# Optimization experiments

Hardware: AMD Instinct MI355X
Metric: run time of the kernel (lower is better)

Reference implementation:

```python
import jax, jax.numpy as jnp
import numpy as np

N = 50000      # nodes
E = 800000     # edges
IN_DIM = 256
H = 128
OUT_DIM = 64
DEPTH = 3
NEG_SLOPE = 0.2  # DGL GATConv default leaky_relu slope


def setup_inputs() -> dict:
    key = jax.random.key(0)
    ks = jax.random.split(key, 20)
    def nrm(k, shape, fan_in):
        return jax.random.normal(k, shape, jnp.float32) / jnp.sqrt(jnp.float32(fan_in))
    x = jax.random.normal(ks[0], (N, IN_DIM), jnp.float32)
    src = jax.random.randint(ks[1], (E,), 0, N, jnp.int32)
    dst = jax.random.randint(ks[2], (E,), 0, N, jnp.int32)
    # weights stored as [in, out] (y = x @ W + b)
    inp = dict(
        x=x, src=src, dst=dst,
        wx_W=nrm(ks[3], (IN_DIM, H), IN_DIM), wx_b=jnp.zeros((H,), jnp.float32),
        gat_W=nrm(ks[4], (DEPTH, H, H), H), gat_b=jnp.zeros((DEPTH, H), jnp.float32),
        attn_l=nrm(ks[5], (DEPTH, H), H), attn_r=nrm(ks[6], (DEPTH, H), H),
        ig_W=nrm(ks[7], (DEPTH, 2 * H, H), 2 * H), ig_b=jnp.zeros((DEPTH, H), jnp.float32),
        fg_W=nrm(ks[8], (DEPTH, 2 * H, H), 2 * H), fg_b=jnp.zeros((DEPTH, H), jnp.float32),
        og_W=nrm(ks[9], (DEPTH, 2 * H, H), 2 * H), og_b=jnp.zeros((DEPTH, H), jnp.float32),
        st_W=nrm(ks[10], (DEPTH, 2 * H, H), 2 * H), st_b=jnp.zeros((DEPTH, H), jnp.float32),
        out_W=nrm(ks[11], (H, OUT_DIM), H), out_b=jnp.zeros((OUT_DIM,), jnp.float32),
    )
    return inp


def _breadth(h, W, b, a_l, a_r, src, dst):
    """DGL GATConv with 1 head + tanh activation; mean over heads is identity."""
    z = h @ W                                  # [N, H]
    el = z @ a_l                               # [N]
    er = z @ a_r                               # [N]
    e = jax.nn.leaky_relu(el[src] + er[dst], NEG_SLOPE)   # [E]
    # edge softmax over incoming edges of each dst node
    emax = jax.ops.segment_max(e, dst, num_segments=N)    # [N]
    emax = jnp.where(jnp.isfinite(emax), emax, 0.0)       # guard isolated nodes
    ex = jnp.exp(e - emax[dst])                            # [E]
    denom = jax.ops.segment_sum(ex, dst, num_segments=N)   # [N]
    alpha = ex / jnp.maximum(denom, 1e-16)[dst]             # [E]
    agg = jax.ops.segment_sum(alpha[:, None] * z[src], dst, num_segments=N)  # [N, H]
    return jnp.tanh(agg + b)


def reference(x, src, dst, wx_W, wx_b, gat_W, gat_b, attn_l, attn_r,
              ig_W, ig_b, fg_W, fg_b, og_W, og_b, st_W, st_b, out_W, out_b):
    h0 = x @ wx_W + wx_b                       # [N, H]
    h = h0
    collector = []
    for i in range(DEPTH):
        h = _breadth(h, gat_W[i], gat_b[i], attn_l[i], attn_r[i], src, dst)
        collector.append(h)
    mu = h0
    c = jnp.zeros_like(mu)
    for i in range(DEPTH):
        hm = jnp.concatenate([collector[i], mu], axis=1)   # [N, 2H]
        ig = jax.nn.sigmoid(hm @ ig_W[i] + ig_b[i])
        fg = jax.nn.sigmoid(hm @ fg_W[i] + fg_b[i])
        og = jax.nn.sigmoid(hm @ og_W[i] + og_b[i])
        c_tilde = jnp.tanh(hm @ st_W[i] + st_b[i])
        c = fg * c + ig * c_tilde
        mu = og * jnp.tanh(c)
    return jax.nn.relu(mu @ out_W + out_b)     # [N, OUT_DIM]
```

## Files before the change

kernel.cpp:

```cpp
#include <hip/hip_runtime.h>
#include <math.h>
#include <type_traits>

#define NN 50000
#define EE 800000
#define IN_D 256
#define HH 128
#define OUT_D 64
#define DEPTH 3
#define BK 512
#define NBK 98

typedef unsigned short u16;
typedef __bf16  bf16x8 __attribute__((ext_vector_type(8)));
typedef short   short8 __attribute__((ext_vector_type(8)));
typedef float   f32x4  __attribute__((ext_vector_type(4)));

__device__ __forceinline__ u16 f2b(float f){
    unsigned u = __float_as_uint(f);
    u += 0x7fff + ((u>>16)&1);
    return (u16)(u>>16);
}
__device__ __forceinline__ float b2f(u16 h){ return __uint_as_float(((unsigned)h)<<16); }

#define LOG2E 1.4426950408889634f
#if __has_builtin(__builtin_amdgcn_exp2f)
__device__ __forceinline__ float fexp2(float x){ return __builtin_amdgcn_exp2f(x); }
#else
__device__ __forceinline__ float fexp2(float x){ return exp2f(x); }
#endif
#if __has_builtin(__builtin_amdgcn_rcpf)
__device__ __forceinline__ float frcp(float x){ return __builtin_amdgcn_rcpf(x); }
#else
__device__ __forceinline__ float frcp(float x){ return 1.f/x; }
#endif
__device__ __forceinline__ float sigm(float x){ return frcp(1.f + fexp2(-x*LOG2E)); }
__device__ __forceinline__ float ftanh(float x){
    float ax = fabsf(x);
    float u = fexp2(ax * (-2.f*LOG2E));
    float r = (1.f - u) * frcp(1.f + u);
    return copysignf(r, x);
}

enum { EPI_BF=0, EPI_RELU=1, EPI_ZEL=2 };

template<int EPI, int WAVES, int CT, int K, typename TA>
__global__ __launch_bounds__(WAVES*64, 4) void rgemm_k(
    const TA* __restrict__ A1,
    const u16* __restrict__ Bp,
    const float* __restrict__ b1, const float* __restrict__ b2,
    void* __restrict__ Out, float* __restrict__ aux1, float* __restrict__ aux2,
    int Nrows)
{
    constexpr int TH = WAVES*64;
    constexpr int KS = K/32;
    constexpr int M  = WAVES*CT*16;
    __shared__ u16 As[64*K];
    __shared__ float elp[(EPI==EPI_ZEL)?64*WAVES:1];
    __shared__ float erp[(EPI==EPI_ZEL)?64*WAVES:1];

    const int tid = threadIdx.x;
    const int rb  = blockIdx.x*64;

    constexpr int CHUNKS = 64*K/(TH*8);
    #pragma unroll
    for (int c = 0; c < CHUNKS; ++c) {
        int h = (tid + c*TH)*8;
        int row = h / K, kk = h % K;
        int grow = rb + row; if (grow >= Nrows) grow = Nrows-1;
        short8 v;
        if constexpr (std::is_same<TA,float>::value) {
            const float* p = (const float*)A1 + (size_t)grow*K + kk;
            float4 x0 = *(const float4*)p;
            float4 x1 = *(const float4*)(p+4);
            v[0]=(short)f2b(x0.x); v[1]=(short)f2b(x0.y); v[2]=(short)f2b(x0.z); v[3]=(short)f2b(x0.w);
            v[4]=(short)f2b(x1.x); v[5]=(short)f2b(x1.y); v[6]=(short)f2b(x1.z); v[7]=(short)f2b(x1.w);
        } else {
            v = *(const short8*)((const u16*)A1 + (size_t)grow*K + kk);
        }
        int byte = row*(K*2) + ((kk*2) ^ ((row&7)<<4));
        *(short8*)((char*)As + byte) = v;
    }
    __syncthreads();

    const int lane = tid & 63, w = tid >> 6;
    const int ml = lane & 15, ksel = lane >> 4;
    f32x4 acc[4][CT] = {};
    #pragma unroll
    for (int ks = 0; ks < KS; ++ks) {
        bf16x8 a[4];
        #pragma unroll
        for (int rt = 0; rt < 4; ++rt) {
            int row = rt*16 + ml;
            int byte = row*(K*2) + (((ks*32 + ksel*8)*2) ^ ((row&7)<<4));
            a[rt] = *(const bf16x8*)((const char*)As + byte);
        }
        #pragma unroll
        for (int j = 0; j < CT; ++j) {
            int ctg = j*WAVES + w;
            bf16x8 b = *(const bf16x8*)(Bp + (((size_t)(ctg*KS + ks))<<9) + lane*8);
            #pragma unroll
            for (int rt = 0; rt < 4; ++rt)
                acc[rt][j] = __builtin_amdgcn_mfma_f32_16x16x32_bf16(a[rt], b, acc[rt][j], 0,0,0);
        }
    }

    if constexpr (EPI==EPI_BF || EPI==EPI_RELU) {
        #pragma unroll
        for (int rt = 0; rt < 4; ++rt)
        #pragma unroll
        for (int r = 0; r < 4; ++r) {
            int row = rb + rt*16 + ksel*4 + r;
            if (row >= Nrows) continue;
            #pragma unroll
            for (int j = 0; j < CT; ++j) {
                int gc = (j*WAVES + w)*16 + ml;
                float vv = acc[rt][j][r] + b1[gc];
                if (EPI==EPI_BF) ((u16*)Out)[(size_t)row*M + gc]   = f2b(vv);
                else             ((float*)Out)[(size_t)row*M + gc] = fmaxf(vv, 0.f);
            }
        }
    } else {
        float pel[4][4] = {}, per[4][4] = {};
        #pragma unroll
        for (int j = 0; j < CT; ++j) {
            int gc = (j*WAVES + w)*16 + ml;
            float alc = b1[gc], arc = b2[gc];
            #pragma unroll
            for (int rt = 0; rt < 4; ++rt)
            #pragma unroll
            for (int r = 0; r < 4; ++r) {
                int row = rb + rt*16 + ksel*4 + r;
                float vv = acc[rt][j][r];
                if (row < Nrows) ((u16*)Out)[(size_t)row*HH + gc] = f2b(vv);
                pel[rt][r] = fmaf(vv, alc, pel[rt][r]);
                per[rt][r] = fmaf(vv, arc, per[rt][r]);
            }
        }
        #pragma unroll
        for (int msk = 1; msk < 16; msk <<= 1)
            #pragma unroll
            for (int rt = 0; rt < 4; ++rt)
            #pragma unroll
            for (int r = 0; r < 4; ++r) {
                pel[rt][r] += __shfl_xor(pel[rt][r], msk);
                per[rt][r] += __shfl_xor(per[rt][r], msk);
            }
        if (ml == 0) {
            #pragma unroll
            for (int rt = 0; rt < 4; ++rt)
            #pragma unroll
            for (int r = 0; r < 4; ++r) {
                int lr = rt*16 + ksel*4 + r;
                elp[lr*WAVES + w] = pel[rt][r];
                erp[lr*WAVES + w] = per[rt][r];
            }
        }
        __syncthreads();
        if (tid < 64) {
            int row = rb + tid;
            if (row < Nrows) {
                float s1 = 0.f, s2 = 0.f;
                #pragma unroll
                for (int wv = 0; wv < WAVES; ++wv) { s1 += elp[tid*WAVES+wv]; s2 += erp[tid*WAVES+wv]; }
                aux1[row] = s1; aux2[row] = s2;
            }
        }
    }
}

__global__ __launch_bounds__(512, 3) void depth_k(
    const u16* __restrict__ coll0, const u16* __restrict__ coll1, const u16* __restrict__ coll2,
    const u16* __restrict__ mu0,
    const u16* __restrict__ gateP, const u16* __restrict__ outP,
    const float* __restrict__ igb, const float* __restrict__ stb,
    const float* __restrict__ fgb, const float* __restrict__ ogb,
    const float* __restrict__ outb, float* __restrict__ Out,
    int Nrows)
{
    __shared__ u16 As[64*HH];
    __shared__ u16 Ms[64*HH];
    const int tid = threadIdx.x;
    const int rb  = blockIdx.x*64;
    const int lane = tid & 63, w = tid >> 6;
    const int ml = lane & 15, ksel = lane >> 4;
    const int gcg = w*16 + ml;

    const int h0_ = tid*8,        h1_ = (tid+512)*8;
    const int row0 = h0_ >> 7,    kk0 = h0_ & 127;
    const int row1 = h1_ >> 7,    kk1 = h1_ & 127;
    int gr0 = rb + row0; if (gr0 >= Nrows) gr0 = Nrows-1;
    int gr1 = rb + row1; if (gr1 >= Nrows) gr1 = Nrows-1;
    const size_t off0 = (size_t)gr0*HH + kk0, off1 = (size_t)gr1*HH + kk1;
    const int dst0 = row0*256 + ((kk0*2) ^ ((row0&7)<<4));
    const int dst1 = row1*256 + ((kk1*2) ^ ((row1&7)<<4));

    *(short8*)((char*)Ms + dst0) = *(const short8*)(mu0 + off0);
    *(short8*)((char*)Ms + dst1) = *(const short8*)(mu0 + off1);
    short8 pf0 = *(const short8*)(coll0 + off0);
    short8 pf1 = *(const short8*)(coll0 + off1);

    float cc[4][4];
    #pragma unroll
    for (int i = 0; i < DEPTH; ++i) {
        __syncthreads();
        *(short8*)((char*)As + dst0) = pf0;
        *(short8*)((char*)As + dst1) = pf1;
        if (i == 0) { pf0 = *(const short8*)(coll1 + off0); pf1 = *(const short8*)(coll1 + off1); }
        if (i == 1) { pf0 = *(const short8*)(coll2 + off0); pf1 = *(const short8*)(coll2 + off1); }
        __syncthreads();

        f32x4 acc[4][4] = {};
        #pragma unroll
        for (int ks = 0; ks < 8; ++ks) {
            const char* Sb = (ks < 4) ? (const char*)As : (const char*)Ms;
            int kk2 = ((ks & 3)*32 + ksel*8)*2;
            bf16x8 a[4];
            #pragma unroll
            for (int rt = 0; rt < 4; ++rt) {
                int row = rt*16 + ml;
                a[rt] = *(const bf16x8*)(Sb + row*256 + (kk2 ^ ((row&7)<<4)));
            }
            #pragma unroll
            for (int g = 0; g < 4; ++g) {
                bf16x8 b = *(const bf16x8*)(gateP + (size_t)i*131072 + (g*8 + w)*4096 + ks*512 + lane*8);
                #pragma unroll
                for (int rt = 0; rt < 4; ++rt)
                    acc[rt][g] = __builtin_amdgcn_mfma_f32_16x16x32_bf16(a[rt], b, acc[rt][g], 0,0,0);
            }
        }
        __syncthreads();

        float bi = igb[i*HH + gcg], bs = stb[i*HH + gcg];
        float bf_ = fgb[i*HH + gcg], bo = ogb[i*HH + gcg];
        #pragma unroll
        for (int rt = 0; rt < 4; ++rt)
        #pragma unroll
        for (int r = 0; r < 4; ++r) {
            float ig = sigm (acc[rt][0][r] + bi);
            float st = ftanh(acc[rt][1][r] + bs);
            float fg = sigm (acc[rt][2][r] + bf_);
            float og = sigm (acc[rt][3][r] + bo);
            float P  = ig * st;
            float cn = (i == 0) ? P : fmaf(fg, cc[rt][r], P);
            cc[rt][r] = cn;
            float mun = og * ftanh(cn);
            int lrow = rt*16 + ksel*4 + r;
            *(u16*)((char*)Ms + lrow*256 + ((gcg*2) ^ ((lrow&7)<<4))) = f2b(mun);
        }
    }
    __syncthreads();

    {
        const int ct = w & 3;
        const int rh = (w >> 2) * 2;
        f32x4 acc[2] = {};
        #pragma unroll
        for (int ks = 0; ks < 4; ++ks) {
            int kk2 = (ks*32 + ksel*8)*2;
            bf16x8 a[2];
            #pragma unroll
            for (int q = 0; q < 2; ++q) {
                int row = (rh + q)*16 + ml;
                a[q] = *(const bf16x8*)((const char*)Ms + row*256 + (kk2 ^ ((row&7)<<4)));
            }
            bf16x8 b = *(const bf16x8*)(outP + (size_t)((ct*4 + ks)<<9) + lane*8);
            #pragma unroll
            for (int q = 0; q < 2; ++q)
                acc[q] = __builtin_amdgcn_mfma_f32_16x16x32_bf16(a[q], b, acc[q], 0,0,0);
        }
        int gc = ct*16 + ml;
        float bb = outb[gc];
        #pragma unroll
        for (int q = 0; q < 2; ++q)
        #pragma unroll
        for (int r = 0; r < 4; ++r) {
            int row = rb + (rh + q)*16 + ksel*4 + r;
            if (row < Nrows)
                Out[(size_t)row*OUT_D + gc] = fmaxf(acc[q][r] + bb, 0.f);
        }
    }
}

struct PK  { const float* s; u16* d; int K; int Mc; };
struct PKs { PK t[17]; };
__global__ __launch_bounds__(256) void pack_k(PKs ps){
    const PK t = ps.t[blockIdx.y];
    int o = blockIdx.x*256 + threadIdx.x;
    if (o >= t.K * t.Mc) return;
    int i = o & 7, lane = (o>>3) & 63, rst = o >> 9;
    int KS = t.K >> 5;
    int ks = rst % KS, ct = rst / KS;
    int col = ct*16 + (lane & 15);
    int k   = ks*32 + (lane>>4)*8 + i;
    t.d[o] = f2b(t.s[(size_t)k*t.Mc + col]);
}

__global__ __launch_bounds__(256) void binh_k(const int* __restrict__ dst, int* __restrict__ bcnt){
    __shared__ int h[NBK];
    int t = threadIdx.x;
    if (t < NBK) h[t] = 0;
    __syncthreads();
    int base = blockIdx.x*4096;
    #pragma unroll
    for (int c = 0; c < 16; ++c){ int e = base + c*256 + t; if (e < EE) atomicAdd(&h[dst[e]>>9], 1); }
    __syncthreads();
    if (t < NBK && h[t]) atomicAdd(&bcnt[t], h[t]);
}
__global__ __launch_bounds__(128) void bscan_k(const int* __restrict__ bcnt,
                                               int* __restrict__ bbase, int* __restrict__ gcur){
    __shared__ int s[128];
    int t = threadIdx.x;
    int v = (t < NBK) ? bcnt[t] : 0;
    s[t] = v; __syncthreads();
    for (int off=1; off<128; off<<=1){ int x = (t>=off)? s[t-off] : 0; __syncthreads(); s[t] += x; __syncthreads(); }
    if (t < NBK){ bbase[t] = s[t]-v; gcur[t] = s[t]-v; }
}
__global__ __launch_bounds__(256) void binsc_k(const int* __restrict__ dst, const int* __restrict__ src,
                                               int* __restrict__ gcur, unsigned* __restrict__ staged){
    __shared__ int h[NBK], bb[NBK], lc[NBK];
    int t = threadIdx.x;
    if (t < NBK){ h[t]=0; lc[t]=0; }
    __syncthreads();
    int base = blockIdx.x*4096;
    int d[16], s[16];
    #pragma unroll
    for (int c = 0; c < 16; ++c){
        int e = base + c*256 + t; d[c] = -1;
        if (e < EE){ d[c] = dst[e]; s[c] = src[e]; atomicAdd(&h[d[c]>>9], 1); }
    }
    __syncthreads();
    if (t < NBK && h[t]) bb[t] = atomicAdd(&gcur[t], h[t]);
    __syncthreads();
    #pragma unroll
    for (int c = 0; c < 16; ++c) if (d[c] >= 0){
        int b = d[c]>>9;
        int r = atomicAdd(&lc[b], 1);
        staged[bb[b] + r] = ((unsigned)(d[c] & 511) << 16) | (unsigned)s[c];
    }
}
__global__ __launch_bounds__(BK) void build_k(const int* __restrict__ bcnt, const int* __restrict__ bbase,
                                              const unsigned* __restrict__ staged,
                                              int* __restrict__ rp, int* __restrict__ deg, u16* __restrict__ srcs){
    __shared__ int soff[BK], cur[BK];
    int t = threadIdx.x, bk = blockIdx.x;
    int n0 = bk*BK;
    soff[t] = 0; cur[t] = 0;
    __syncthreads();
    int cb = bcnt[bk], eb = bbase[bk];
    for (int j = t; j < cb; j += BK) atomicAdd(&soff[staged[eb+j]>>16], 1);
    __syncthreads();
    int d0 = soff[t];
    for (int off=1; off<BK; off<<=1){ int x = (t>=off)? soff[t-off] : 0; __syncthreads(); soff[t] += x; __syncthreads(); }
    int ex = soff[t] - d0;
    __syncthreads();
    soff[t] = ex;
    int n = n0 + t;
    if (n < NN){ deg[n] = d0; rp[n] = eb + ex; }
    __syncthreads();
    for (int j = t; j < cb; j += BK){
        unsigned p = staged[eb+j];
        int l = p >> 16;
        int r = atomicAdd(&cur[l], 1);
        srcs[eb + soff[l] + r] = (u16)(p & 0xffff);
    }
}

__global__ __launch_bounds__(256) void gat_k(
    const u16* __restrict__ z, const float* __restrict__ el, const float* __restrict__ er,
    const u16* __restrict__ srcs, const int* __restrict__ rp, const int* __restrict__ deg,
    const float* __restrict__ bias, u16* __restrict__ hout)
{
    int n = blockIdx.x*4 + (threadIdx.x>>6);
    if (n >= NN) return;
    int lane = threadIdx.x & 63;
    int start = rp[n], cnt = deg[n];
    float ern = er[n];
    const int slot = lane >> 4;
    const int ch   = (lane & 15) * 8;
    float acc[8] = {};

    if (cnt <= 64) {
        float v = -1e30f; int s_reg = 0;
        if (lane < cnt) {
            s_reg = srcs[start + lane];
            float tv = el[s_reg] + ern;
            v = tv >= 0.f ? tv : 0.2f*tv;
        }
        float m = v;
        #pragma unroll
        for (int off=1; off<64; off<<=1) m = fmaxf(m, __shfl_xor(m, off));
        float a = (lane < cnt) ? fexp2((v - m)*LOG2E) : 0.f;
        float ss = a;
        #pragma unroll
        for (int off=1; off<64; off<<=1) ss += __shfl_xor(ss, off);
        float a_reg = a * frcp(fmaxf(ss, 1e-16f));

        const int cntp = (cnt + 7) & ~7;
        for (int i = slot; i < cntp; i += 8) {
            float w0 = __shfl(a_reg, i),   w1 = __shfl(a_reg, i+4);
            int   s0 = __shfl(s_reg, i),   s1 = __shfl(s_reg, i+4);
            short8 v0 = *(const short8*)(z + (size_t)s0*HH + ch);
            short8 v1 = *(const short8*)(z + (size_t)s1*HH + ch);
            #pragma unroll
            for (int j=0;j<8;j++) acc[j] = fmaf(w1, b2f((u16)v1[j]), fmaf(w0, b2f((u16)v0[j]), acc[j]));
        }
    } else {
        float m = -1e30f;
        for (int i=lane; i<cnt; i+=64){ float tv = el[srcs[start+i]] + ern; tv = tv>=0.f?tv:0.2f*tv; m = fmaxf(m, tv); }
        #pragma unroll
        for (int off=1; off<64; off<<=1) m = fmaxf(m, __shfl_xor(m, off));
        float ss = 0.f;
        for (int i=lane; i<cnt; i+=64){ float tv = el[srcs[start+i]] + ern; tv = tv>=0.f?tv:0.2f*tv; ss += fexp2((tv-m)*LOG2E); }
        #pragma unroll
        for (int off=1; off<64; off<<=1) ss += __shfl_xor(ss, off);
        float inv = frcp(fmaxf(ss, 1e-16f));
        for (int i=slot; i<cnt; i+=4) {
            int sn = srcs[start+i];
            float tv = el[sn] + ern; tv = tv>=0.f?tv:0.2f*tv;
            float w0 = fexp2((tv-m)*LOG2E) * inv;
            short8 v0 = *(const short8*)(z + (size_t)sn*HH + ch);
            #pragma unroll
            for (int j=0;j<8;j++) acc[j] = fmaf(w0, b2f((u16)v0[j]), acc[j]);
        }
    }
    #pragma unroll
    for (int j=0;j<8;j++){ acc[j] += __shfl_xor(acc[j],16); acc[j] += __shfl_xor(acc[j],32); }
    if (slot == 0) {
        short8 o8;
        #pragma unroll
        for (int j=0;j<8;j++) o8[j] = (short)f2b(ftanh(acc[j] + bias[ch+j]));
        *(short8*)(hout + (size_t)n*HH + ch) = o8;
    }
}

extern "C" void kernel_launch(void* const* d_in, const int* in_sizes, int n_in,
                              void* d_out, int out_size, void* d_ws, size_t ws_size,
                              hipStream_t stream)
{
    const float* x    = (const float*)d_in[0];
    const int*   src  = (const int*)d_in[1];
    const int*   dst  = (const int*)d_in[2];
    const float* wxW  = (const float*)d_in[3];
    const float* wxb  = (const float*)d_in[4];
    const float* gatW = (const float*)d_in[5];
    const float* gatb = (const float*)d_in[6];
    const float* attl = (const float*)d_in[7];
    const float* attr = (const float*)d_in[8];
    const float* igW  = (const float*)d_in[9];
    const float* igb  = (const float*)d_in[10];
    const float* fgW  = (const float*)d_in[11];
    const float* fgb  = (const float*)d_in[12];
    const float* ogW  = (const float*)d_in[13];
    const float* ogb  = (const float*)d_in[14];
    const float* stW  = (const float*)d_in[15];
    const float* stb  = (const float*)d_in[16];
    const float* outW = (const float*)d_in[17];
    const float* outb = (const float*)d_in[18];

    char* w = (char*)d_ws;
    auto alloc = [&](size_t bytes)->char* { char* p = w; w += (bytes + 255) & ~(size_t)255; return p; };
    const size_t NH = (size_t)NN * HH;
    u16*      muB    = (u16*)alloc(NH*2);
    u16*      zB     = (u16*)alloc(NH*2);
    u16*      coll0  = (u16*)alloc(NH*2);
    u16*      coll1  = (u16*)alloc(NH*2);
    u16*      coll2  = (u16*)alloc(NH*2);
    float*    el     = (float*)alloc((size_t)NN*4);
    float*    er     = (float*)alloc((size_t)NN*4);
    unsigned* staged = (unsigned*)alloc((size_t)EE*4);
    u16*      srcs   = (u16*)alloc((size_t)EE*2);
    int*      deg    = (int*)alloc((size_t)NN*4);
    int*      rp     = (int*)alloc((size_t)NN*4);
    int*      bcnt   = (int*)alloc(128*4);
    int*      bbase  = (int*)alloc(128*4);
    int*      gcur   = (int*)alloc(128*4);
    u16*      bpool  = (u16*)alloc(483328*2);
    u16* wxP   = bpool;
    u16* gatP  = bpool + 32768;
    u16* gateP = bpool + 81920;
    u16* outP  = bpool + 475136;
    u16* coll[3] = {coll0, coll1, coll2};

    PKs ps;
    ps.t[0] = {wxW, wxP, IN_D, HH};
    for (int i=0;i<3;i++) ps.t[1+i]  = {gatW + (size_t)i*HH*HH,   gatP  + i*16384,           HH,   HH};
    for (int i=0;i<3;i++) ps.t[4+i]  = {igW  + (size_t)i*2*HH*HH, gateP + i*131072,          2*HH, HH};
    for (int i=0;i<3;i++) ps.t[7+i]  = {stW  + (size_t)i*2*HH*HH, gateP + i*131072 + 32768,  2*HH, HH};
    for (int i=0;i<3;i++) ps.t[10+i] = {fgW  + (size_t)i*2*HH*HH, gateP + i*131072 + 65536,  2*HH, HH};
    for (int i=0;i<3;i++) ps.t[13+i] = {ogW  + (size_t)i*2*HH*HH, gateP + i*131072 + 98304,  2*HH, HH};
    ps.t[16] = {outW, outP, HH, OUT_D};
    pack_k<<<dim3(128,17), 256, 0, stream>>>(ps);

    hipMemsetAsync(bcnt, 0, 128*4, stream);
    const int gE = (EE + 4095) / 4096;
    binh_k <<<gE, 256, 0, stream>>>(dst, bcnt);
    bscan_k<<<1, 128, 0, stream>>>(bcnt, bbase, gcur);
    binsc_k<<<gE, 256, 0, stream>>>(dst, src, gcur, staged);
    build_k<<<NBK, BK, 0, stream>>>(bcnt, bbase, staged, rp, deg, srcs);

    const int gN = (NN + 63) / 64;
    const int gA = (NN + 3) / 4;

    rgemm_k<EPI_BF,4,2,IN_D,float><<<gN, 256, 0, stream>>>(
        x, wxP, wxb, nullptr, muB, nullptr, nullptr, NN);

    const u16* hin = muB;
    for (int i = 0; i < DEPTH; ++i) {
        rgemm_k<EPI_ZEL,4,2,HH,u16><<<gN, 256, 0, stream>>>(
            hin, gatP + i*16384, attl + i*HH, attr + i*HH, zB, el, er, NN);
        gat_k<<<gA, 256, 0, stream>>>(zB, el, er, srcs, rp, deg, gatb + i*HH, coll[i]);
        hin = coll[i];
    }

    depth_k<<<gN, 512, 0, stream>>>(coll0, coll1, coll2, muB, gateP, outP,
                                    igb, stb, fgb, ogb, outb, (float*)d_out, NN);
}
```

Baseline: 305.2 us.

## Store LDS A tiles in MFMA fragment order and prefetch gate weights

Result: no change. 304.9 us (-0.1%).

```diff
diff --git a/kernel.cpp b/kernel.cpp
--- a/kernel.cpp
+++ b/kernel.cpp
@@ -65,20 +65,20 @@
     constexpr int CHUNKS = 64*K/(TH*8);
     #pragma unroll
     for (int c = 0; c < CHUNKS; ++c) {
-        int h = (tid + c*TH)*8;
-        int row = h / K, kk = h % K;
+        int cidx = tid + c*TH;
+        int row = cidx & 63, kseg = cidx >> 6;
         int grow = rb + row; if (grow >= Nrows) grow = Nrows-1;
         short8 v;
         if constexpr (std::is_same<TA,float>::value) {
-            const float* p = (const float*)A1 + (size_t)grow*K + kk;
+            const float* p = (const float*)A1 + (size_t)grow*K + kseg*8;
             float4 x0 = *(const float4*)p;
             float4 x1 = *(const float4*)(p+4);
             v[0]=(short)f2b(x0.x); v[1]=(short)f2b(x0.y); v[2]=(short)f2b(x0.z); v[3]=(short)f2b(x0.w);
             v[4]=(short)f2b(x1.x); v[5]=(short)f2b(x1.y); v[6]=(short)f2b(x1.z); v[7]=(short)f2b(x1.w);
         } else {
-            v = *(const short8*)((const u16*)A1 + (size_t)grow*K + kk);
-        }
-        int byte = row*(K*2) + ((kk*2) ^ ((row&7)<<4));
+            v = *(const short8*)((const u16*)A1 + (size_t)grow*K + kseg*8);
+        }
+        int byte = ((row>>4)*KS + (kseg>>2))*1024 + ((kseg&3)*16 + (row&15))*16;
         *(short8*)((char*)As + byte) = v;
     }
     __syncthreads();
@@ -90,11 +90,8 @@
     for (int ks = 0; ks < KS; ++ks) {
         bf16x8 a[4];
         #pragma unroll
-        for (int rt = 0; rt < 4; ++rt) {
-            int row = rt*16 + ml;
-            int byte = row*(K*2) + (((ks*32 + ksel*8)*2) ^ ((row&7)<<4));
-            a[rt] = *(const bf16x8*)((const char*)As + byte);
-        }
+        for (int rt = 0; rt < 4; ++rt)
+            a[rt] = *(const bf16x8*)((const char*)As + (rt*KS + ks)*1024 + lane*16);
         #pragma unroll
         for (int j = 0; j < CT; ++j) {
             int ctg = j*WAVES + w;
@@ -186,14 +183,14 @@
     const int ml = lane & 15, ksel = lane >> 4;
     const int gcg = w*16 + ml;
 
-    const int h0_ = tid*8,        h1_ = (tid+512)*8;
-    const int row0 = h0_ >> 7,    kk0 = h0_ & 127;
-    const int row1 = h1_ >> 7,    kk1 = h1_ & 127;
+    const int c0 = tid, c1 = tid + 512;
+    const int row0 = c0 & 63, kg0 = c0 >> 6;
+    const int row1 = c1 & 63, kg1 = c1 >> 6;
     int gr0 = rb + row0; if (gr0 >= Nrows) gr0 = Nrows-1;
     int gr1 = rb + row1; if (gr1 >= Nrows) gr1 = Nrows-1;
-    const size_t off0 = (size_t)gr0*HH + kk0, off1 = (size_t)gr1*HH + kk1;
-    const int dst0 = row0*256 + ((kk0*2) ^ ((row0&7)<<4));
-    const int dst1 = row1*256 + ((kk1*2) ^ ((row1&7)<<4));
+    const size_t off0 = (size_t)gr0*HH + kg0*8, off1 = (size_t)gr1*HH + kg1*8;
+    const int dst0 = ((row0>>4)*4 + (kg0>>2))*1024 + ((kg0&3)*16 + (row0&15))*16;
+    const int dst1 = ((row1>>4)*4 + (kg1>>2))*1024 + ((kg1&3)*16 + (row1&15))*16;
 
     *(short8*)((char*)Ms + dst0) = *(const short8*)(mu0 + off0);
     *(short8*)((char*)Ms + dst1) = *(const short8*)(mu0 + off1);
@@ -211,28 +208,40 @@
         __syncthreads();
 
         f32x4 acc[4][4] = {};
+        bf16x8 bc[4];
+        #pragma unroll
+        for (int g = 0; g < 4; ++g)
+            bc[g] = *(const bf16x8*)(gateP + (size_t)i*131072 + (g*8 + w)*4096 + lane*8);
         #pragma unroll
         for (int ks = 0; ks < 8; ++ks) {
+            bf16x8 bn[4];
+            if (ks < 7) {
+                #pragma unroll
+                for (int g = 0; g < 4; ++g)
+                    bn[g] = *(const bf16x8*)(gateP + (size_t)i*131072 + (g*8 + w)*4096 + (ks+1)*512 + lane*8);
+            }
             const char* Sb = (ks < 4) ? (const char*)As : (const char*)Ms;
-            int kk2 = ((ks & 3)*32 + ksel*8)*2;
             bf16x8 a[4];
             #pragma unroll
-            for (int rt = 0; rt < 4; ++rt) {
-                int row = rt*16 + ml;
-                a[rt] = *(const bf16x8*)(Sb + row*256 + (kk2 ^ ((row&7)<<4)));
-            }
-            #pragma unroll
-            for (int g = 0; g < 4; ++g) {
-                bf16x8 b = *(const bf16x8*)(gateP + (size_t)i*131072 + (g*8 + w)*4096 + ks*512 + lane*8);
+            for (int rt = 0; rt < 4; ++rt)
+                a[rt] = *(const bf16x8*)(Sb + (rt*4 + (ks&3))*1024 + lane*16);
+            #pragma unroll
+            for (int g = 0; g < 4; ++g)
                 #pragma unroll
                 for (int rt = 0; rt < 4; ++rt)
-                    acc[rt][g] = __builtin_amdgcn_mfma_f32_16x16x32_bf16(a[rt], b, acc[rt][g], 0,0,0);
+                    acc[rt][g] = __builtin_amdgcn_mfma_f32_16x16x32_bf16(a[rt], bc[g], acc[rt][g], 0,0,0);
+            if (ks < 7) {
+                #pragma unroll
+                for (int g = 0; g < 4; ++g) bc[g] = bn[g];
             }
         }
         __syncthreads();
 
         float bi = igb[i*HH + gcg], bs = stb[i*HH + gcg];
         float bf_ = fgb[i*HH + gcg], bo = ogb[i*HH + gcg];
+        const int fks  = gcg >> 5;
+        const int shi  = (gcg >> 3) & 3;
+        const int elem = gcg & 7;
         #pragma unroll
         for (int rt = 0; rt < 4; ++rt)
         #pragma unroll
@@ -245,8 +254,8 @@
             float cn = (i == 0) ? P : fmaf(fg, cc[rt][r], P);
             cc[rt][r] = cn;
             float mun = og * ftanh(cn);
-            int lrow = rt*16 + ksel*4 + r;
-            *(u16*)((char*)Ms + lrow*256 + ((gcg*2) ^ ((lrow&7)<<4))) = f2b(mun);
+            int byte = (rt*4 + fks)*1024 + (shi*16 + (ksel*4 + r))*16 + elem*2;
+            *(u16*)((char*)Ms + byte) = f2b(mun);
         }
     }
     __syncthreads();
@@ -257,13 +266,10 @@
         f32x4 acc[2] = {};
         #pragma unroll
         for (int ks = 0; ks < 4; ++ks) {
-            int kk2 = (ks*32 + ksel*8)*2;
             bf16x8 a[2];
             #pragma unroll
-            for (int q = 0; q < 2; ++q) {
-                int row = (rh + q)*16 + ml;
-                a[q] = *(const bf16x8*)((const char*)Ms + row*256 + (kk2 ^ ((row&7)<<4)));
-            }
+            for (int q = 0; q < 2; ++q)
+                a[q] = *(const bf16x8*)((const char*)Ms + ((rh+q)*4 + ks)*1024 + lane*16);
             bf16x8 b = *(const bf16x8*)(outP + (size_t)((ct*4 + ks)<<9) + lane*8);
             #pragma unroll
             for (int q = 0; q < 2; ++q)
```
